# Optimization experiments

Hardware: AMD Instinct MI355X
Metric: run time of the kernel (lower is better)

Reference implementation:

```python
import jax, jax.numpy as jnp
import numpy as np

B, N, F_IN, F, H, K = 4, 128, 16, 64, 4, 50
C = F * H            # n_coefficients = hidden * n_heads
DEPTH, STEPS = 2, 3
L = 2 * DEPTH        # stacked flow layers: [xv0, vx0, xv1, vx1]
EPS = 1e-5

PARAM_NAMES = ["emb1_w", "emb1_b", "emb2_w", "emb2_b",
               "edge_in_w", "edge_in_b", "rbf_means", "rbf_betas",
               "edge_out1_w", "edge_out1_b", "edge_out2_w", "edge_out2_b",
               "xmix_w", "post1_w", "post1_b", "post2_w", "post2_b",
               "sem_w", "sem_b", "node1_w", "node1_b", "node2_w", "node2_b",
               "vel1_w", "vel1_b", "vel2_w", "coord1_w", "coord1_b", "coord2_w"]


def _lin(x, w, b=None):
    y = x @ w
    return y if b is None else y + b


def _pair_cat(h):
    # h_cat_ht: [B,N,N,2F], entry (i,j) = concat(h_i, h_j)
    return jnp.concatenate([jnp.broadcast_to(h[:, :, None, :], (B, N, N, F)),
                            jnp.broadcast_to(h[:, None, :, :], (B, N, N, F))], -1)


def _mp(p, i, h, x):
    dx = x[:, :, None, :] - x[:, None, :, :]                       # [B,N,N,3] x_i - x_j
    dn = jnp.sqrt(jnp.sum(dx * dx, -1, keepdims=True) + EPS * EPS)  # [B,N,N,1]
    hh = _pair_cat(h)                                              # [B,N,N,2F]
    # edge model: continuous-filter conv with concatenation (ExpNormal RBF smearing)
    hk = _lin(hh, p["edge_in_w"][i], p["edge_in_b"][i])            # [B,N,N,K]
    smear = jnp.exp(-p["rbf_betas"][i] * (jnp.exp(-dn) - p["rbf_means"][i]) ** 2)
    z = jnp.concatenate([hh, smear * hk, dn], -1)                  # [B,N,N,2F+K+1]
    he = _lin(jax.nn.silu(_lin(z, p["edge_out1_w"][i], p["edge_out1_b"][i])),
              p["edge_out2_w"][i], p["edge_out2_b"][i])            # [B,N,N,F]
    # spatial attention: mix unit displacement vectors with learned coefficients
    coeff = jnp.tanh(_lin(he, p["xmix_w"][i]))                     # [B,N,N,C]
    dxu = dx / (dn + EPS)
    comb = jnp.einsum('bijd,bijc->bicd', dxu, coeff) / N           # mean over j, [B,N,C,3]
    hc = jax.nn.silu(_lin(jnp.sum(comb * comb, -1), p["post1_w"][i], p["post1_b"][i]))
    hc = jax.nn.silu(_lin(hc, p["post2_w"][i], p["post2_b"][i]))   # [B,N,F]
    # semantic multi-head attention over neighbors j (self-edge masked)
    logits = jax.nn.celu(_lin(he, p["sem_w"][i], p["sem_b"][i]), alpha=2.0)  # [B,N,N,H]
    eye = jnp.eye(N, dtype=logits.dtype)[None, :, :, None]
    att = jax.nn.softmax(logits - 1e5 * eye, axis=-2)              # normalize over j
    # (h_e_mtx[...,None] * att[...,None,:]).flatten(-2,-1).sum(-2) without [B,N,N,F*H]
    h_e = jnp.einsum('bijf,bijh->bifh', he, att).reshape(B, N, C)  # [B,N,C]
    z = jnp.concatenate([h, h_e, hc], -1)                          # [B,N,F+C+F]
    out = jax.nn.silu(_lin(z, p["node1_w"][i], p["node1_b"][i]))
    out = jax.nn.silu(_lin(out, p["node2_w"][i], p["node2_b"][i]))
    return h + out                                                 # residual node update


def _flow(p, i, h, x, v):
    for _ in range(STEPS):
        h = _mp(p, i, h, x)
    hh = _pair_cat(h)
    dx = x[:, :, None, :] - x[:, None, :, :]
    c = _lin(jax.nn.silu(_lin(hh, p["coord1_w"][i], p["coord1_b"][i])), p["coord2_w"][i])
    delta_v = jnp.mean(c * dx, axis=-2)                            # [B,N,3]
    m = _lin(jax.nn.silu(_lin(h, p["vel1_w"][i], p["vel1_b"][i])), p["vel2_w"][i])  # [B,N,1]
    v = jnp.exp(m) * v
    log_det = jnp.sum(m, (-1, -2)) * 3.0                           # * v.shape[-1]
    v = delta_v + v
    x = x + v
    return x, v, log_det


def _forward(h, x, v, params):
    p = dict(zip(PARAM_NAMES, params))
    h = _lin(jax.nn.silu(_lin(h, p["emb1_w"], p["emb1_b"])), p["emb2_w"], p["emb2_b"])
    sld = jnp.zeros((B,), h.dtype)
    for d in range(DEPTH):
        x, v, ld = _flow(p, 2 * d, h, x, v)
        x = x - x.mean(-2, keepdims=True)
        v = v - v.mean(-2, keepdims=True)
        sld = sld + ld
        v, x, ld = _flow(p, 2 * d + 1, h, v, x)   # roles of x and v swapped
        x = x - x.mean(-2, keepdims=True)
        v = v - v.mean(-2, keepdims=True)
        sld = sld + ld
    return x, v, sld


def setup_inputs() -> dict:
    key = jax.random.key(0)
    ki = iter(jax.random.split(key, 40))
    def W(shape):
        fan = shape[-2] if len(shape) >= 2 else shape[-1]
        return jax.random.normal(next(ki), shape, jnp.float32) / np.float32(np.sqrt(fan))
    def Z(shape):
        return jnp.zeros(shape, jnp.float32)
    inp = {
        "h": jax.random.normal(next(ki), (B, N, F_IN), jnp.float32),
        "x": jax.random.normal(next(ki), (B, N, 3), jnp.float32),
        "v": jax.random.normal(next(ki), (B, N, 3), jnp.float32),
        "emb1_w": W((F_IN, F)), "emb1_b": Z((F,)),
        "emb2_w": W((F, F)), "emb2_b": Z((F,)),
        "edge_in_w": W((L, 2 * F, K)), "edge_in_b": Z((L, K)),
        "rbf_means": jnp.tile(jnp.linspace(np.float32(np.exp(-5.0)), 1.0, K, dtype=jnp.float32)[None], (L, 1)),
        "rbf_betas": jnp.full((L, K), np.float32(((2.0 / K) * (1.0 - np.exp(-5.0))) ** -2), jnp.float32),
        "edge_out1_w": W((L, 2 * F + K + 1, F)), "edge_out1_b": Z((L, F)),
        "edge_out2_w": W((L, F, F)), "edge_out2_b": Z((L, F)),
        "xmix_w": W((L, F, C)),
        "post1_w": W((L, C, F)), "post1_b": Z((L, F)),
        "post2_w": W((L, F, F)), "post2_b": Z((L, F)),
        "sem_w": W((L, F, H)), "sem_b": Z((L, H)),
        "node1_w": W((L, F + C + F, F)), "node1_b": Z((L, F)),
        "node2_w": W((L, F, F)), "node2_b": Z((L, F)),
        "vel1_w": W((L, F, F)), "vel1_b": Z((L, F)),
        "vel2_w": W((L, F, 1)),
        "coord1_w": W((L, 2 * F, F)), "coord1_b": Z((L, F)),
        "coord2_w": W((L, F, 1)),
    }
    return inp


def reference(h, x, v, emb1_w, emb1_b, emb2_w, emb2_b, edge_in_w, edge_in_b,
              rbf_means, rbf_betas, edge_out1_w, edge_out1_b, edge_out2_w, edge_out2_b,
              xmix_w, post1_w, post1_b, post2_w, post2_b, sem_w, sem_b,
              node1_w, node1_b, node2_w, node2_b, vel1_w, vel1_b, vel2_w,
              coord1_w, coord1_b, coord2_w):
    params = (emb1_w, emb1_b, emb2_w, emb2_b, edge_in_w, edge_in_b, rbf_means, rbf_betas,
              edge_out1_w, edge_out1_b, edge_out2_w, edge_out2_b, xmix_w,
              post1_w, post1_b, post2_w, post2_b, sem_w, sem_b,
              node1_w, node1_b, node2_w, node2_b, vel1_w, vel1_b, vel2_w,
              coord1_w, coord1_b, coord2_w)
    return _forward(h, x, v, params)
```

## Files before the change

### kernel.cpp

```cpp
#include <hip/hip_runtime.h>
#include <math.h>

namespace {

constexpr int B = 4, N = 128, FIN = 16, F = 64, H = 4, K = 50, C = 256;
constexpr int BN = B * N;
constexpr float EPS = 1e-5f;

typedef float v2f __attribute__((ext_vector_type(2)));
__device__ __forceinline__ v2f mk2(float a, float b) { v2f r; r.x = a; r.y = b; return r; }

__device__ __forceinline__ float silu_f(float x) { return x / (1.0f + __expf(-x)); }
__device__ __forceinline__ float tanh_f(float x) { return 1.0f - 2.0f / (__expf(2.0f * x) + 1.0f); }

__global__ void k_init(const float* __restrict__ x, const float* __restrict__ v,
                       float* __restrict__ xw, float* __restrict__ vw, float* __restrict__ sld) {
  int t = blockIdx.x * blockDim.x + threadIdx.x;
  if (t < B * N * 3) { xw[t] = x[t]; vw[t] = v[t]; }
  if (t < B) sld[t] = 0.0f;
}

__global__ __launch_bounds__(F) void k_embed(const float* __restrict__ hin,
    const float* __restrict__ w1, const float* __restrict__ b1,
    const float* __restrict__ w2, const float* __restrict__ b2, float* __restrict__ h0) {
  int node = blockIdx.x, f = threadIdx.x;
  __shared__ float t1[F];
  float acc = b1[f];
  #pragma unroll
  for (int r = 0; r < FIN; ++r) acc += hin[node * FIN + r] * w1[r * F + f];
  t1[f] = silu_f(acc);
  __syncthreads();
  float a0 = b2[f], a1 = 0.f, a2 = 0.f, a3 = 0.f;
  #pragma unroll
  for (int r = 0; r < F; r += 4) {
    a0 += t1[r] * w2[r * F + f];
    a1 += t1[r + 1] * w2[(r + 1) * F + f];
    a2 += t1[r + 2] * w2[(r + 2) * F + f];
    a3 += t1[r + 3] * w2[(r + 3) * F + f];
  }
  h0[node * F + f] = (a0 + a1) + (a2 + a3);
}

__global__ __launch_bounds__(256) void k_pre(const float* __restrict__ h0, float* __restrict__ hw,
    const float* __restrict__ ein_w, const float* __restrict__ eo1w,
    float* __restrict__ hkA, float* __restrict__ hkB,
    float* __restrict__ e1A, float* __restrict__ e1B) {
  int node = blockIdx.x, t = threadIdx.x;
  __shared__ float s_h[F];
  if (t < F) s_h[t] = h0[node * F + t];
  __syncthreads();
  if (t < F) hw[node * F + t] = s_h[t];
  if (t < 228) {
    v2f pa = mk2(0.f, 0.f), pb = mk2(0.f, 0.f);
    if (t < 50) { int k = t;
      #pragma unroll
      for (int r = 0; r < F; r += 4) {
        pa += mk2(s_h[r], s_h[r + 1]) * mk2(ein_w[r * K + k], ein_w[(r + 1) * K + k]);
        pb += mk2(s_h[r + 2], s_h[r + 3]) * mk2(ein_w[(r + 2) * K + k], ein_w[(r + 3) * K + k]);
      }
      hkA[node * K + k] = (pa.x + pb.x) + (pa.y + pb.y);
    } else if (t < 100) { int k = t - 50;
      #pragma unroll
      for (int r = 0; r < F; r += 4) {
        pa += mk2(s_h[r], s_h[r + 1]) * mk2(ein_w[(F + r) * K + k], ein_w[(F + r + 1) * K + k]);
        pb += mk2(s_h[r + 2], s_h[r + 3]) * mk2(ein_w[(F + r + 2) * K + k], ein_w[(F + r + 3) * K + k]);
      }
      hkB[node * K + k] = (pa.x + pb.x) + (pa.y + pb.y);
    } else if (t < 164) { int c = t - 100;
      #pragma unroll
      for (int r = 0; r < F; r += 4) {
        pa += mk2(s_h[r], s_h[r + 1]) * mk2(eo1w[r * F + c], eo1w[(r + 1) * F + c]);
        pb += mk2(s_h[r + 2], s_h[r + 3]) * mk2(eo1w[(r + 2) * F + c], eo1w[(r + 3) * F + c]);
      }
      e1A[node * F + c] = (pa.x + pb.x) + (pa.y + pb.y);
    } else { int c = t - 164;
      #pragma unroll
      for (int r = 0; r < F; r += 4) {
        pa += mk2(s_h[r], s_h[r + 1]) * mk2(eo1w[(F + r) * F + c], eo1w[(F + r + 1) * F + c]);
        pb += mk2(s_h[r + 2], s_h[r + 3]) * mk2(eo1w[(F + r + 2) * F + c], eo1w[(F + r + 3) * F + c]);
      }
      e1B[node * F + c] = (pa.x + pb.x) + (pa.y + pb.y);
    }
  }
}

__global__ __launch_bounds__(256, 2) void k_edge(
    const float* __restrict__ xp,
    const float* __restrict__ hkA_in, const float* __restrict__ hkB_in,
    const float* __restrict__ e1A_in, const float* __restrict__ e1B_in,
    const float* __restrict__ ein_b, const float* __restrict__ rbf_m, const float* __restrict__ rbf_b,
    const float* __restrict__ eo1w, const float* __restrict__ eo1b,
    const float* __restrict__ eo2w, const float* __restrict__ eo2b,
    const float* __restrict__ xmix,
    const float* __restrict__ semw, const float* __restrict__ semb,
    float* __restrict__ mS, float* __restrict__ Upart, float* __restrict__ combpart) {
  int blk = blockIdx.x;
  int b = blk >> 8, i = (blk >> 1) & 127, jh = blk & 1;
  int t = threadIdx.x, w = t >> 6, lane = t & 63;
  int bN = b * N;
  int bi2 = ((bN + i) << 1) + jh;

  __shared__ __align__(16) float s_heT[64 * 68];
  __shared__ __align__(16) float s_union[4352];
  __shared__ __align__(16) float4 s_dxn[64];
  __shared__ float s_inv[64];
  __shared__ float s_zkbase[K];
  __shared__ float s_e1base[F];
  __shared__ __align__(16) float s_zk[4][2][56];

  float* t1buf   = s_union;
  float* s_cpart = s_union;
  float* s_att   = s_union + 3072;

  if (t < K) s_zkbase[t] = hkA_in[(bN + i) * K + t] + ein_b[t];
  if (t >= 64 && t < 128) s_e1base[t - 64] = e1A_in[(bN + i) * F + (t - 64)] + eo1b[t - 64];
  if (lane >= 50 && lane < 56) { s_zk[w][0][lane] = 0.f; s_zk[w][1][lane] = 0.f; }
  if (t < 64) {
    const float* xb_ = xp + bN * 3;
    int jg = jh * 64 + t;
    float dx0 = xb_[i * 3 + 0] - xb_[jg * 3 + 0];
    float dx1 = xb_[i * 3 + 1] - xb_[jg * 3 + 1];
    float dx2 = xb_[i * 3 + 2] - xb_[jg * 3 + 2];
    float dn = sqrtf(dx0 * dx0 + dx1 * dx1 + dx2 * dx2 + EPS * EPS);
    s_dxn[t] = make_float4(dx0, dx1, dx2, dn);
    s_inv[t] = 1.0f / (dn + EPS);
  }
  __syncthreads();

  float rbm = 0.f, rbb = 0.f;
  if (lane < K) { rbm = rbf_m[lane]; rbb = rbf_b[lane]; }

  {
    int jbl = w * 16;
    int jbg = jh * 64 + jbl;
    {
      v2f wk2[26];
      #pragma unroll
      for (int k = 0; k < 25; ++k)
        wk2[k] = mk2(eo1w[(128 + 2 * k) * F + lane], eo1w[(128 + 2 * k + 1) * F + lane]);
      wk2[25] = mk2(0.f, 0.f);
      float w1d = eo1w[178 * F + lane];
      float e1b_lane = s_e1base[lane];
      float hk0 = (lane < K) ? hkB_in[(bN + jbg) * K + lane] : 0.f;
      float e1_c = e1B_in[(bN + jbg) * F + lane];
      if (lane < K) {
        float dn0 = s_dxn[jbl].w;
        float e = __expf(-dn0) - rbm;
        s_zk[w][0][lane] = __expf(-rbb * e * e) * (s_zkbase[lane] + hk0);
      }
      float hk_n = (lane < K) ? hkB_in[(bN + jbg + 1) * K + lane] : 0.f;
      float e1_n = e1B_in[(bN + jbg + 1) * F + lane];
      for (int jj = 0; jj < 16; ++jj) {
        int jl = jbl + jj;
        int cur = jj & 1;
        if (jj < 15) {
          if (lane < K) {
            float dn1 = s_dxn[jl + 1].w;
            float e = __expf(-dn1) - rbm;
            s_zk[w][cur ^ 1][lane] = __expf(-rbb * e * e) * (s_zkbase[lane] + hk_n);
          }
        }
        float e1v = e1_c;
        if (jj < 14) {
          hk_n = (lane < K) ? hkB_in[(bN + jbg + jj + 2) * K + lane] : 0.f;
          e1_c = e1_n;
          e1_n = e1B_in[(bN + jbg + jj + 2) * F + lane];
        } else {
          e1_c = e1_n;
        }
        float dn = s_dxn[jl].w;
        v2f pa = mk2(0.f, 0.f), pb = mk2(0.f, 0.f);
        const float4* z4 = (const float4*)(&s_zk[w][cur][0]);
        #pragma unroll
        for (int k4 = 0; k4 < 13; ++k4) {
          float4 z = z4[k4];
          pa += mk2(z.x, z.y) * wk2[2 * k4];
          pb += mk2(z.z, z.w) * wk2[2 * k4 + 1];
        }
        float base_ = e1b_lane + e1v + dn * w1d;
        float sum = base_ + ((pa.x + pb.x) + (pa.y + pb.y));
        t1buf[jl * 68 + lane] = silu_f(sum);
      }
    }
    {
      v2f er2[32];
      #pragma unroll
      for (int r = 0; r < 32; ++r)
        er2[r] = mk2(eo2w[(2 * r) * F + lane], eo2w[(2 * r + 1) * F + lane]);
      float b2 = eo2b[lane];
      for (int jj4 = 0; jj4 < 4; ++jj4) {
        float hv[4];
        #pragma unroll
        for (int q = 0; q < 4; ++q) {
          const float4* t4 = (const float4*)(&t1buf[(jbl + jj4 * 4 + q) * 68]);
          v2f pa = mk2(0.f, 0.f), pb = mk2(0.f, 0.f);
          #pragma unroll
          for (int r4 = 0; r4 < 16; ++r4) {
            float4 tt = t4[r4];
            pa += mk2(tt.x, tt.y) * er2[2 * r4];
            pb += mk2(tt.z, tt.w) * er2[2 * r4 + 1];
          }
          hv[q] = b2 + ((pa.x + pb.x) + (pa.y + pb.y));
        }
        *(float4*)(&s_heT[lane * 68 + jbl + jj4 * 4]) = make_float4(hv[0], hv[1], hv[2], hv[3]);
      }
    }
  }
  __syncthreads();

  {
    int c0 = 4 * (t & 63);
    v2f aX = mk2(0.f, 0.f), aXh = mk2(0.f, 0.f);
    v2f aY = mk2(0.f, 0.f), aYh = mk2(0.f, 0.f);
    v2f aZ = mk2(0.f, 0.f), aZh = mk2(0.f, 0.f);
    #pragma unroll 1
    for (int p = 0; p < 2; ++p) {
      int j0 = w * 16 + p * 8;
      v2f caccL[8], caccH[8];
      #pragma unroll
      for (int jj = 0; jj < 8; ++jj) { caccL[jj] = mk2(0.f, 0.f); caccH[jj] = mk2(0.f, 0.f); }
      for (int r = 0; r < 64; ++r) {
        float4 xm4 = *(const float4*)(&xmix[r * C + c0]);
        v2f xmL = mk2(xm4.x, xm4.y), xmH = mk2(xm4.z, xm4.w);
        const float4* hb = (const float4*)(&s_heT[r * 68 + j0]);
        float4 h0v = hb[0], h1v = hb[1];
#define CSTEP(idx, hval) \
        caccL[idx] += xmL * (hval); caccH[idx] += xmH * (hval);
        CSTEP(0, h0v.x)  CSTEP(1, h0v.y)  CSTEP(2, h0v.z)  CSTEP(3, h0v.w)
        CSTEP(4, h1v.x)  CSTEP(5, h1v.y)  CSTEP(6, h1v.z)  CSTEP(7, h1v.w)
#undef CSTEP
      }
      #pragma unroll
      for (int jj = 0; jj < 8; ++jj) {
        int jl = j0 + jj;
        float4 dq = s_dxn[jl];
        float inv = s_inv[jl];
        float s0 = tanh_f(caccL[jj].x) * inv;
        float s1 = tanh_f(caccL[jj].y) * inv;
        float s2 = tanh_f(caccH[jj].x) * inv;
        float s3 = tanh_f(caccH[jj].y) * inv;
        v2f s01 = mk2(s0, s1), s23 = mk2(s2, s3);
        aX  += s01 * dq.x; aXh += s23 * dq.x;
        aY  += s01 * dq.y; aYh += s23 * dq.y;
        aZ  += s01 * dq.z; aZh += s23 * dq.z;
      }
    }
    int cb = w * 768 + c0 * 3;
    s_cpart[cb + 0] = aX.x;  s_cpart[cb + 1]  = aY.x;  s_cpart[cb + 2]  = aZ.x;
    s_cpart[cb + 3] = aX.y;  s_cpart[cb + 4]  = aY.y;  s_cpart[cb + 5]  = aZ.y;
    s_cpart[cb + 6] = aXh.x; s_cpart[cb + 7]  = aYh.x; s_cpart[cb + 8]  = aZh.x;
    s_cpart[cb + 9] = aXh.y; s_cpart[cb + 10] = aYh.y; s_cpart[cb + 11] = aZh.y;
  }
  __syncthreads();

  {
    int c = t;
    float q0 = s_cpart[c * 3 + 0] + s_cpart[768 + c * 3 + 0] + s_cpart[1536 + c * 3 + 0] + s_cpart[2304 + c * 3 + 0];
    float q1 = s_cpart[c * 3 + 1] + s_cpart[768 + c * 3 + 1] + s_cpart[1536 + c * 3 + 1] + s_cpart[2304 + c * 3 + 1];
    float q2 = s_cpart[c * 3 + 2] + s_cpart[768 + c * 3 + 2] + s_cpart[1536 + c * 3 + 2] + s_cpart[2304 + c * 3 + 2];
    combpart[bi2 * 768 + c * 3 + 0] = q0;
    combpart[bi2 * 768 + c * 3 + 1] = q1;
    combpart[bi2 * 768 + c * 3 + 2] = q2;
  }

  {
    int jl = t & 63, hh = w;
    int jg = jh * 64 + jl;
    v2f lacc = mk2(0.f, 0.f);
    #pragma unroll 8
    for (int r = 0; r < 64; r += 2) {
      float hv0 = s_heT[r * 68 + jl];
      float hv1 = s_heT[(r + 1) * 68 + jl];
      lacc += mk2(hv0, hv1) * mk2(semw[r * H + hh], semw[(r + 1) * H + hh]);
    }
    float lg = semb[hh] + lacc.x + lacc.y;
    lg = lg > 0.f ? lg : 2.0f * (__expf(0.5f * lg) - 1.0f);
    if (jg == i) lg -= 1e5f;
    float m = lg;
    #pragma unroll
    for (int off = 32; off > 0; off >>= 1) m = fmaxf(m, __shfl_xor(m, off));
    float e = __expf(lg - m);
    float S = e;
    #pragma unroll
    for (int off = 32; off > 0; off >>= 1) S += __shfl_xor(S, off);
    s_att[hh * 64 + jl] = e;
    if (lane == 0) { mS[bi2 * 8 + hh * 2] = m; mS[bi2 * 8 + hh * 2 + 1] = S; }
  }
  __syncthreads();

  {
    int f = t >> 2, hh = t & 3;
    const float4* hr = (const float4*)(&s_heT[f * 68]);
    const float4* ar = (const float4*)(&s_att[hh * 64]);
    v2f pa = mk2(0.f, 0.f), pb = mk2(0.f, 0.f);
    #pragma unroll 8
    for (int jg4 = 0; jg4 < 16; ++jg4) {
      float4 hv = hr[jg4];
      float4 av = ar[jg4];
      pa += mk2(hv.x, hv.y) * mk2(av.x, av.y);
      pb += mk2(hv.z, hv.w) * mk2(av.z, av.w);
    }
    Upart[bi2 * 256 + t] = (pa.x + pb.x) + (pa.y + pb.y);
  }
}

template<int PRE, int TAIL>
__global__ __launch_bounds__(256, 2) void k_comb(
    float* __restrict__ hw,
    const float* __restrict__ mS, const float* __restrict__ Upart, const float* __restrict__ combpart,
    const float* __restrict__ p1w, const float* __restrict__ p1b,
    const float* __restrict__ p2w, const float* __restrict__ p2b,
    const float* __restrict__ n1w, const float* __restrict__ n1b,
    const float* __restrict__ n2w, const float* __restrict__ n2b,
    const float* __restrict__ ein_w, const float* __restrict__ eo1w,
    float* __restrict__ hkA_out, float* __restrict__ hkB_out,
    float* __restrict__ e1A_out, float* __restrict__ e1B_out,
    const float* __restrict__ c1w, const float* __restrict__ v1w, const float* __restrict__ v1b,
    const float* __restrict__ v2w,
    float* __restrict__ uA, float* __restrict__ uB, float* __restrict__ mbuf) {
  int blk = blockIdx.x, b = blk >> 7, i = blk & 127;
  int t = threadIdx.x, w = t >> 6, lane = t & 63;
  int bN = b * N;
  int bi2 = (bN + i) << 1;
  constexpr float invN = 1.0f / (float)N;

  __shared__ float s_hcin[C];
  __shared__ float s_cat[384];
  __shared__ float s_part[4][F];
  __shared__ float s_vec[F];
  __shared__ float s_hnew[F];

  float hi_val = (t < F) ? hw[(bN + i) * F + t] : 0.f;

  {
    int hh = t & 3;
    float m0 = mS[bi2 * 8 + hh * 2],       S0 = mS[bi2 * 8 + hh * 2 + 1];
    float m1 = mS[(bi2 + 1) * 8 + hh * 2], S1 = mS[(bi2 + 1) * 8 + hh * 2 + 1];
    float m = fmaxf(m0, m1);
    float w0 = __expf(m0 - m), w1 = __expf(m1 - m);
    float u = w0 * Upart[bi2 * 256 + t] + w1 * Upart[(bi2 + 1) * 256 + t];
    s_cat[64 + t] = u / (w0 * S0 + w1 * S1);
  }
  {
    int c = t;
    float q0 = (combpart[bi2 * 768 + c * 3 + 0] + combpart[(bi2 + 1) * 768 + c * 3 + 0]) * invN;
    float q1 = (combpart[bi2 * 768 + c * 3 + 1] + combpart[(bi2 + 1) * 768 + c * 3 + 1]) * invN;
    float q2 = (combpart[bi2 * 768 + c * 3 + 2] + combpart[(bi2 + 1) * 768 + c * 3 + 2]) * invN;
    s_hcin[c] = q0 * q0 + q1 * q1 + q2 * q2;
  }
  __syncthreads();

  {
    int c0 = w * 64;
    v2f pa = mk2(0.f, 0.f), pb = mk2(0.f, 0.f);
    #pragma unroll 8
    for (int cc = 0; cc < 64; cc += 4) {
      pa += mk2(s_hcin[c0 + cc], s_hcin[c0 + cc + 1])
          * mk2(p1w[(c0 + cc) * F + lane], p1w[(c0 + cc + 1) * F + lane]);
      pb += mk2(s_hcin[c0 + cc + 2], s_hcin[c0 + cc + 3])
          * mk2(p1w[(c0 + cc + 2) * F + lane], p1w[(c0 + cc + 3) * F + lane]);
    }
    s_part[w][lane] = (pa.x + pb.x) + (pa.y + pb.y);
  }
  __syncthreads();
  if (t < F) s_vec[t] = silu_f(s_part[0][t] + s_part[1][t] + s_part[2][t] + s_part[3][t] + p1b[t]);
  __syncthreads();
  if (t < F) {
    v2f pa = mk2(0.f, 0.f), pb = mk2(0.f, 0.f);
    #pragma unroll 8
    for (int r = 0; r < F; r += 4) {
      pa += mk2(s_vec[r], s_vec[r + 1]) * mk2(p2w[r * F + t], p2w[(r + 1) * F + t]);
      pb += mk2(s_vec[r + 2], s_vec[r + 3]) * mk2(p2w[(r + 2) * F + t], p2w[(r + 3) * F + t]);
    }
    s_cat[t] = hi_val;
    s_cat[320 + t] = silu_f(p2b[t] + (pa.x + pb.x) + (pa.y + pb.y));
  }
  __syncthreads();
  {
    int r0 = w * 96;
    v2f pa = mk2(0.f, 0.f), pb = mk2(0.f, 0.f);
    #pragma unroll 8
    for (int rr = 0; rr < 96; rr += 4) {
      pa += mk2(s_cat[r0 + rr], s_cat[r0 + rr + 1])
          * mk2(n1w[(r0 + rr) * F + lane], n1w[(r0 + rr + 1) * F + lane]);
      pb += mk2(s_cat[r0 + rr + 2], s_cat[r0 + rr + 3])
          * mk2(n1w[(r0 + rr + 2) * F + lane], n1w[(r0 + rr + 3) * F + lane]);
    }
    s_part[w][lane] = (pa.x + pb.x) + (pa.y + pb.y);
  }
  __syncthreads();
  if (t < F) s_vec[t] = silu_f(s_part[0][t] + s_part[1][t] + s_part[2][t] + s_part[3][t] + n1b[t]);
  __syncthreads();
  if (t < F) {
    v2f pa = mk2(0.f, 0.f), pb = mk2(0.f, 0.f);
    #pragma unroll 8
    for (int r = 0; r < F; r += 4) {
      pa += mk2(s_vec[r], s_vec[r + 1]) * mk2(n2w[r * F + t], n2w[(r + 1) * F + t]);
      pb += mk2(s_vec[r + 2], s_vec[r + 3]) * mk2(n2w[(r + 2) * F + t], n2w[(r + 3) * F + t]);
    }
    float hn = hi_val + silu_f(n2b[t] + (pa.x + pb.x) + (pa.y + pb.y));
    s_hnew[t] = hn;
    hw[(bN + i) * F + t] = hn;
  }
  __syncthreads();

  if (PRE) {
    if (t < 228) {
      v2f pa = mk2(0.f, 0.f), pb = mk2(0.f, 0.f);
      if (t < 50) { int k = t;
        #pragma unroll
        for (int r = 0; r < F; r += 4) {
          pa += mk2(s_hnew[r], s_hnew[r + 1]) * mk2(ein_w[r * K + k], ein_w[(r + 1) * K + k]);
          pb += mk2(s_hnew[r + 2], s_hnew[r + 3]) * mk2(ein_w[(r + 2) * K + k], ein_w[(r + 3) * K + k]);
        }
        hkA_out[(bN + i) * K + k] = (pa.x + pb.x) + (pa.y + pb.y);
      } else if (t < 100) { int k = t - 50;
        #pragma unroll
        for (int r = 0; r < F; r += 4) {
          pa += mk2(s_hnew[r], s_hnew[r + 1]) * mk2(ein_w[(F + r) * K + k], ein_w[(F + r + 1) * K + k]);
          pb += mk2(s_hnew[r + 2], s_hnew[r + 3]) * mk2(ein_w[(F + r + 2) * K + k], ein_w[(F + r + 3) * K + k]);
        }
        hkB_out[(bN + i) * K + k] = (pa.x + pb.x) + (pa.y + pb.y);
      } else if (t < 164) { int c = t - 100;
        #pragma unroll
        for (int r = 0; r < F; r += 4) {
          pa += mk2(s_hnew[r], s_hnew[r + 1]) * mk2(eo1w[r * F + c], eo1w[(r + 1) * F + c]);
          pb += mk2(s_hnew[r + 2], s_hnew[r + 3]) * mk2(eo1w[(r + 2) * F + c], eo1w[(r + 3) * F + c]);
        }
        e1A_out[(bN + i) * F + c] = (pa.x + pb.x) + (pa.y + pb.y);
      } else { int c = t - 164;
        #pragma unroll
        for (int r = 0; r < F; r += 4) {
          pa += mk2(s_hnew[r], s_hnew[r + 1]) * mk2(eo1w[(F + r) * F + c], eo1w[(F + r + 1) * F + c]);
          pb += mk2(s_hnew[r + 2], s_hnew[r + 3]) * mk2(eo1w[(F + r + 2) * F + c], eo1w[(F + r + 3) * F + c]);
        }
        e1B_out[(bN + i) * F + c] = (pa.x + pb.x) + (pa.y + pb.y);
      }
    }
  }
  if (TAIL) {
    if (w == 0) {
      v2f pa = mk2(0.f, 0.f), pb = mk2(0.f, 0.f);
      #pragma unroll
      for (int r = 0; r < F; r += 4) {
        pa += mk2(s_hnew[r], s_hnew[r + 1]) * mk2(c1w[r * F + lane], c1w[(r + 1) * F + lane]);
        pb += mk2(s_hnew[r + 2], s_hnew[r + 3]) * mk2(c1w[(r + 2) * F + lane], c1w[(r + 3) * F + lane]);
      }
      uA[(bN + i) * F + lane] = (pa.x + pb.x) + (pa.y + pb.y);
    } else if (w == 1) {
      v2f pa = mk2(0.f, 0.f), pb = mk2(0.f, 0.f);
      #pragma unroll
      for (int r = 0; r < F; r += 4) {
        pa += mk2(s_hnew[r], s_hnew[r + 1]) * mk2(c1w[(F + r) * F + lane], c1w[(F + r + 1) * F + lane]);
        pb += mk2(s_hnew[r + 2], s_hnew[r + 3]) * mk2(c1w[(F + r + 2) * F + lane], c1w[(F + r + 3) * F + lane]);
      }
      uB[(bN + i) * F + lane] = (pa.x + pb.x) + (pa.y + pb.y);
    } else if (w == 2) {
      v2f pa = mk2(0.f, 0.f), pb = mk2(0.f, 0.f);
      #pragma unroll
      for (int r = 0; r < F; r += 4) {
        pa += mk2(s_hnew[r], s_hnew[r + 1]) * mk2(v1w[r * F + lane], v1w[(r + 1) * F + lane]);
        pb += mk2(s_hnew[r + 2], s_hnew[r + 3]) * mk2(v1w[(r + 2) * F + lane], v1w[(r + 3) * F + lane]);
      }
      float tv = silu_f(v1b[lane] + (pa.x + pb.x) + (pa.y + pb.y)) * v2w[lane];
      #pragma unroll
      for (int off = 32; off > 0; off >>= 1) tv += __shfl_down(tv, off);
      if (lane == 0) mbuf[bN + i] = tv;
    }
  }
}

__global__ __launch_bounds__(256) void k_tail(const float* __restrict__ xb,
    const float* __restrict__ uA, const float* __restrict__ uB,
    const float* __restrict__ c1b, const float* __restrict__ c2w,
    float* __restrict__ dv) {
  int blk = blockIdx.x, b = blk >> 7, i = blk & 127;
  int t = threadIdx.x, w = t >> 6, lane = t & 63;
  __shared__ float s_xpos[N * 3];
  __shared__ float s_uAi[F];
  __shared__ float s_acc[4][3];
  for (int idx = t; idx < N * 3; idx += 256) s_xpos[idx] = xb[b * N * 3 + idx];
  if (t < F) s_uAi[t] = uA[(b * N + i) * F + t];
  __syncthreads();
  float xi0 = s_xpos[i * 3 + 0], xi1 = s_xpos[i * 3 + 1], xi2 = s_xpos[i * 3 + 2];
  float base = s_uAi[lane] + c1b[lane];
  float c2v = c2w[lane];
  float a0 = 0.f, a1 = 0.f, a2 = 0.f;
  for (int jj = 0; jj < 32; ++jj) {
    int j = w + 4 * jj;
    float tv = silu_f(base + uB[(b * N + j) * F + lane]) * c2v;
    #pragma unroll
    for (int off = 32; off > 0; off >>= 1) tv += __shfl_down(tv, off);
    if (lane == 0) {
      float dx0 = xi0 - s_xpos[j * 3 + 0];
      float dx1 = xi1 - s_xpos[j * 3 + 1];
      float dx2 = xi2 - s_xpos[j * 3 + 2];
      a0 += tv * dx0; a1 += tv * dx1; a2 += tv * dx2;
    }
  }
  if (lane == 0) { s_acc[w][0] = a0; s_acc[w][1] = a1; s_acc[w][2] = a2; }
  __syncthreads();
  if (t < 3) {
    float s = s_acc[0][t] + s_acc[1][t] + s_acc[2][t] + s_acc[3][t];
    dv[(b * N + i) * 3 + t] = s * (1.0f / (float)N);
  }
}

__global__ __launch_bounds__(128) void k_fin(float* __restrict__ xb, float* __restrict__ vb,
    const float* __restrict__ dv, const float* __restrict__ mbuf, float* __restrict__ sld) {
  int b = blockIdx.x, t = threadIdx.x;
  __shared__ float red[N];
  float m = mbuf[b * N + t];
  float em = __expf(m);
  float vv[3], xx[3];
  #pragma unroll
  for (int d = 0; d < 3; ++d) {
    int idx = (b * N + t) * 3 + d;
    vv[d] = em * vb[idx] + dv[idx];
    xx[d] = xb[idx] + vv[d];
  }
  #pragma unroll
  for (int d = 0; d < 3; ++d) {
    red[t] = xx[d];
    __syncthreads();
    for (int s = 64; s > 0; s >>= 1) { if (t < s) red[t] += red[t + s]; __syncthreads(); }
    xx[d] -= red[0] * (1.0f / (float)N);
    __syncthreads();
    red[t] = vv[d];
    __syncthreads();
    for (int s = 64; s > 0; s >>= 1) { if (t < s) red[t] += red[t + s]; __syncthreads(); }
    vv[d] -= red[0] * (1.0f / (float)N);
    __syncthreads();
  }
  #pragma unroll
  for (int d = 0; d < 3; ++d) {
    int idx = (b * N + t) * 3 + d;
    xb[idx] = xx[d];
    vb[idx] = vv[d];
  }
  red[t] = m;
  __syncthreads();
  for (int s = 64; s > 0; s >>= 1) { if (t < s) red[t] += red[t + s]; __syncthreads(); }
  if (t == 0) sld[b] += 3.0f * red[0];
}

__global__ void k_out(const float* __restrict__ xw, const float* __restrict__ vw,
                      const float* __restrict__ sld, float* __restrict__ out) {
  int t = blockIdx.x * blockDim.x + threadIdx.x;
  if (t < B * N * 3) { out[t] = xw[t]; out[B * N * 3 + t] = vw[t]; }
  if (t < B) out[2 * B * N * 3 + t] = sld[t];
}

}

extern "C" void kernel_launch(void* const* d_in, const int* in_sizes, int n_in,
                              void* d_out, int out_size, void* d_ws, size_t ws_size,
                              hipStream_t stream) {
  const float* in_h   = (const float*)d_in[0];
  const float* in_x   = (const float*)d_in[1];
  const float* in_v   = (const float*)d_in[2];
  const float* emb1_w = (const float*)d_in[3];
  const float* emb1_b = (const float*)d_in[4];
  const float* emb2_w = (const float*)d_in[5];
  const float* emb2_b = (const float*)d_in[6];
  const float* ein_w  = (const float*)d_in[7];
  const float* ein_b  = (const float*)d_in[8];
  const float* rbf_m  = (const float*)d_in[9];
  const float* rbf_b  = (const float*)d_in[10];
  const float* eo1w   = (const float*)d_in[11];
  const float* eo1b   = (const float*)d_in[12];
  const float* eo2w   = (const float*)d_in[13];
  const float* eo2b   = (const float*)d_in[14];
  const float* xmix   = (const float*)d_in[15];
  const float* p1w    = (const float*)d_in[16];
  const float* p1b    = (const float*)d_in[17];
  const float* p2w    = (const float*)d_in[18];
  const float* p2b    = (const float*)d_in[19];
  const float* semw   = (const float*)d_in[20];
  const float* semb   = (const float*)d_in[21];
  const float* n1w    = (const float*)d_in[22];
  const float* n1b    = (const float*)d_in[23];
  const float* n2w    = (const float*)d_in[24];
  const float* n2b    = (const float*)d_in[25];
  const float* v1w    = (const float*)d_in[26];
  const float* v1b    = (const float*)d_in[27];
  const float* v2w    = (const float*)d_in[28];
  const float* c1w    = (const float*)d_in[29];
  const float* c1b    = (const float*)d_in[30];
  const float* c2w    = (const float*)d_in[31];

  float* ws   = (float*)d_ws;
  float* h0   = ws;
  float* hw   = h0 + BN * F;
  float* hkA0 = hw + BN * F;
  float* hkB0 = hkA0 + BN * K;
  float* e1A0 = hkB0 + BN * K;
  float* e1B0 = e1A0 + BN * F;
  float* hkA1 = e1B0 + BN * F;
  float* hkB1 = hkA1 + BN * K;
  float* e1A1 = hkB1 + BN * K;
  float* e1B1 = e1A1 + BN * F;
  float* uA   = e1B1 + BN * F;
  float* uB   = uA + BN * F;
  float* xw   = uB + BN * F;
  float* vw   = xw + BN * 3;
  float* dvb  = vw + BN * 3;
  float* mbuf = dvb + BN * 3;
  float* sld  = mbuf + BN;
  float* mS   = sld + B;
  float* Up   = mS + BN * 2 * 8;
  float* cp   = Up + BN * 2 * 256;

  k_init<<<6, 256, 0, stream>>>(in_x, in_v, xw, vw, sld);
  k_embed<<<BN, F, 0, stream>>>(in_h, emb1_w, emb1_b, emb2_w, emb2_b, h0);

  float* hkA[2] = {hkA0, hkA1};
  float* hkB[2] = {hkB0, hkB1};
  float* e1A[2] = {e1A0, e1A1};
  float* e1B[2] = {e1B0, e1B1};

  for (int dep = 0; dep < 2; ++dep) {
    for (int half = 0; half < 2; ++half) {
      int l = 2 * dep + half;
      float* xb = half ? vw : xw;
      float* vb = half ? xw : vw;
      const float* einw_l = ein_w + l * 2 * F * K;
      const float* einb_l = ein_b + l * K;
      const float* rbm_l  = rbf_m + l * K;
      const float* rbb_l  = rbf_b + l * K;
      const float* eo1w_l = eo1w + l * 179 * F;
      const float* eo1b_l = eo1b + l * F;
      const float* eo2w_l = eo2w + l * F * F;
      const float* eo2b_l = eo2b + l * F;
      const float* xmix_l = xmix + l * F * C;
      const float* p1w_l  = p1w + l * C * F;
      const float* p1b_l  = p1b + l * F;
      const float* p2w_l  = p2w + l * F * F;
      const float* p2b_l  = p2b + l * F;
      const float* semw_l = semw + l * F * H;
      const float* semb_l = semb + l * H;
      const float* n1w_l  = n1w + l * 384 * F;
      const float* n1b_l  = n1b + l * F;
      const float* n2w_l  = n2w + l * F * F;
      const float* n2b_l  = n2b + l * F;
      const float* v1w_l  = v1w + l * F * F;
      const float* v1b_l  = v1b + l * F;
      const float* v2w_l  = v2w + l * F;
      const float* c1w_l  = c1w + l * 2 * F * F;
      const float* c1b_l  = c1b + l * F;
      const float* c2w_l  = c2w + l * F;

      k_pre<<<BN, 256, 0, stream>>>(h0, hw, einw_l, eo1w_l, hkA[0], hkB[0], e1A[0], e1B[0]);
      k_edge<<<BN * 2, 256, 0, stream>>>(xb, hkA[0], hkB[0], e1A[0], e1B[0],
          einb_l, rbm_l, rbb_l, eo1w_l, eo1b_l, eo2w_l, eo2b_l, xmix_l, semw_l, semb_l,
          mS, Up, cp);
      k_comb<1, 0><<<BN, 256, 0, stream>>>(hw, mS, Up, cp,
          p1w_l, p1b_l, p2w_l, p2b_l, n1w_l, n1b_l, n2w_l, n2b_l,
          einw_l, eo1w_l, hkA[1], hkB[1], e1A[1], e1B[1],
          c1w_l, v1w_l, v1b_l, v2w_l, uA, uB, mbuf);
      k_edge<<<BN * 2, 256, 0, stream>>>(xb, hkA[1], hkB[1], e1A[1], e1B[1],
          einb_l, rbm_l, rbb_l, eo1w_l, eo1b_l, eo2w_l, eo2b_l, xmix_l, semw_l, semb_l,
          mS, Up, cp);
      k_comb<1, 0><<<BN, 256, 0, stream>>>(hw, mS, Up, cp,
          p1w_l, p1b_l, p2w_l, p2b_l, n1w_l, n1b_l, n2w_l, n2b_l,
          einw_l, eo1w_l, hkA[0], hkB[0], e1A[0], e1B[0],
          c1w_l, v1w_l, v1b_l, v2w_l, uA, uB, mbuf);
      k_edge<<<BN * 2, 256, 0, stream>>>(xb, hkA[0], hkB[0], e1A[0], e1B[0],
          einb_l, rbm_l, rbb_l, eo1w_l, eo1b_l, eo2w_l, eo2b_l, xmix_l, semw_l, semb_l,
          mS, Up, cp);
      k_comb<0, 1><<<BN, 256, 0, stream>>>(hw, mS, Up, cp,
          p1w_l, p1b_l, p2w_l, p2b_l, n1w_l, n1b_l, n2w_l, n2b_l,
          einw_l, eo1w_l, hkA[1], hkB[1], e1A[1], e1B[1],
          c1w_l, v1w_l, v1b_l, v2w_l, uA, uB, mbuf);
      k_tail<<<BN, 256, 0, stream>>>(xb, uA, uB, c1b_l, c2w_l, dvb);
      k_fin<<<B, 128, 0, stream>>>(xb, vb, dvb, mbuf, sld);
    }
  }
  k_out<<<6, 256, 0, stream>>>(xw, vw, sld, (float*)d_out);
}
```

Measured before the change: 916.6 us.

## Split edge kernel over four j-quarters per node instead of two

```diff
diff --git a/kernel.cpp b/kernel.cpp
--- a/kernel.cpp
+++ b/kernel.cpp
@@ -95,29 +95,30 @@
     const float* __restrict__ semw, const float* __restrict__ semb,
     float* __restrict__ mS, float* __restrict__ Upart, float* __restrict__ combpart) {
   int blk = blockIdx.x;
-  int b = blk >> 8, i = (blk >> 1) & 127, jh = blk & 1;
+  int b = blk >> 9, i = (blk >> 2) & 127, jq = blk & 3;
   int t = threadIdx.x, w = t >> 6, lane = t & 63;
   int bN = b * N;
-  int bi2 = ((bN + i) << 1) + jh;
-
-  __shared__ __align__(16) float s_heT[64 * 68];
-  __shared__ __align__(16) float s_union[4352];
-  __shared__ __align__(16) float4 s_dxn[64];
-  __shared__ float s_inv[64];
+  int bi4 = ((bN + i) << 2) + jq;
+  int jgbase = jq * 32;
+
+  __shared__ __align__(16) float s_heT[64 * 36];
+  __shared__ __align__(16) float s_union[2176];
+  __shared__ __align__(16) float4 s_dxn[32];
+  __shared__ float s_inv[32];
   __shared__ float s_zkbase[K];
   __shared__ float s_e1base[F];
-  __shared__ __align__(16) float s_zk[4][2][56];
-
-  float* t1buf   = s_union;
-  float* s_cpart = s_union;
-  float* s_att   = s_union + 3072;
+  __shared__ __align__(16) float s_zk[4][56];
+
+  float* t1buf  = s_union;
+  float* s_comb = s_union;
+  float* s_att  = s_union + 768;
 
   if (t < K) s_zkbase[t] = hkA_in[(bN + i) * K + t] + ein_b[t];
   if (t >= 64 && t < 128) s_e1base[t - 64] = e1A_in[(bN + i) * F + (t - 64)] + eo1b[t - 64];
-  if (lane >= 50 && lane < 56) { s_zk[w][0][lane] = 0.f; s_zk[w][1][lane] = 0.f; }
-  if (t < 64) {
+  if (lane >= 50 && lane < 56) s_zk[w][lane] = 0.f;
+  if (t < 32) {
     const float* xb_ = xp + bN * 3;
-    int jg = jh * 64 + t;
+    int jg = jgbase + t;
     float dx0 = xb_[i * 3 + 0] - xb_[jg * 3 + 0];
     float dx1 = xb_[i * 3 + 1] - xb_[jg * 3 + 1];
     float dx2 = xb_[i * 3 + 2] - xb_[jg * 3 + 2];
@@ -131,8 +132,8 @@
   if (lane < K) { rbm = rbf_m[lane]; rbb = rbf_b[lane]; }
 
   {
-    int jbl = w * 16;
-    int jbg = jh * 64 + jbl;
+    int jbl = w * 8;
+    int nb = bN + jgbase + jbl;
     {
       v2f wk2[26];
       #pragma unroll
@@ -141,45 +142,31 @@
       wk2[25] = mk2(0.f, 0.f);
       float w1d = eo1w[178 * F + lane];
       float e1b_lane = s_e1base[lane];
-      float hk0 = (lane < K) ? hkB_in[(bN + jbg) * K + lane] : 0.f;
-      float e1_c = e1B_in[(bN + jbg) * F + lane];
-      if (lane < K) {
-        float dn0 = s_dxn[jbl].w;
-        float e = __expf(-dn0) - rbm;
-        s_zk[w][0][lane] = __expf(-rbb * e * e) * (s_zkbase[lane] + hk0);
-      }
-      float hk_n = (lane < K) ? hkB_in[(bN + jbg + 1) * K + lane] : 0.f;
-      float e1_n = e1B_in[(bN + jbg + 1) * F + lane];
-      for (int jj = 0; jj < 16; ++jj) {
+      float hk_c = (lane < K) ? hkB_in[nb * K + lane] : 0.f;
+      float e1_c = e1B_in[nb * F + lane];
+      for (int jj = 0; jj < 8; ++jj) {
         int jl = jbl + jj;
-        int cur = jj & 1;
-        if (jj < 15) {
-          if (lane < K) {
-            float dn1 = s_dxn[jl + 1].w;
-            float e = __expf(-dn1) - rbm;
-            s_zk[w][cur ^ 1][lane] = __expf(-rbb * e * e) * (s_zkbase[lane] + hk_n);
-          }
-        }
-        float e1v = e1_c;
-        if (jj < 14) {
-          hk_n = (lane < K) ? hkB_in[(bN + jbg + jj + 2) * K + lane] : 0.f;
-          e1_c = e1_n;
-          e1_n = e1B_in[(bN + jbg + jj + 2) * F + lane];
-        } else {
-          e1_c = e1_n;
+        float hk_n = 0.f, e1_n = 0.f;
+        if (jj < 7) {
+          hk_n = (lane < K) ? hkB_in[(nb + jj + 1) * K + lane] : 0.f;
+          e1_n = e1B_in[(nb + jj + 1) * F + lane];
         }
         float dn = s_dxn[jl].w;
+        if (lane < K) {
+          float e = __expf(-dn) - rbm;
+          s_zk[w][lane] = __expf(-rbb * e * e) * (s_zkbase[lane] + hk_c);
+        }
         v2f pa = mk2(0.f, 0.f), pb = mk2(0.f, 0.f);
-        const float4* z4 = (const float4*)(&s_zk[w][cur][0]);
+        const float4* z4 = (const float4*)(&s_zk[w][0]);
         #pragma unroll
         for (int k4 = 0; k4 < 13; ++k4) {
           float4 z = z4[k4];
           pa += mk2(z.x, z.y) * wk2[2 * k4];
           pb += mk2(z.z, z.w) * wk2[2 * k4 + 1];
         }
-        float base_ = e1b_lane + e1v + dn * w1d;
-        float sum = base_ + ((pa.x + pb.x) + (pa.y + pb.y));
-        t1buf[jl * 68 + lane] = silu_f(sum);
+        float base_ = e1b_lane + e1_c + dn * w1d;
+        t1buf[jl * 68 + lane] = silu_f(base_ + ((pa.x + pb.x) + (pa.y + pb.y)));
+        hk_c = hk_n; e1_c = e1_n;
       }
     }
     {
@@ -188,7 +175,7 @@
       for (int r = 0; r < 32; ++r)
         er2[r] = mk2(eo2w[(2 * r) * F + lane], eo2w[(2 * r + 1) * F + lane]);
       float b2 = eo2b[lane];
-      for (int jj4 = 0; jj4 < 4; ++jj4) {
+      for (int jj4 = 0; jj4 < 2; ++jj4) {
         float hv[4];
         #pragma unroll
         for (int q = 0; q < 4; ++q) {
@@ -202,75 +189,70 @@
           }
           hv[q] = b2 + ((pa.x + pb.x) + (pa.y + pb.y));
         }
-        *(float4*)(&s_heT[lane * 68 + jbl + jj4 * 4]) = make_float4(hv[0], hv[1], hv[2], hv[3]);
-      }
-    }
-  }
+        *(float4*)(&s_heT[lane * 36 + jbl + jj4 * 4]) = make_float4(hv[0], hv[1], hv[2], hv[3]);
+      }
+    }
+  }
+  __syncthreads();
+  for (int idx = t; idx < 768; idx += 256) s_comb[idx] = 0.f;
   __syncthreads();
 
   {
     int c0 = 4 * (t & 63);
+    int j0 = w * 8;
+    v2f caccL[8], caccH[8];
+    #pragma unroll
+    for (int jj = 0; jj < 8; ++jj) { caccL[jj] = mk2(0.f, 0.f); caccH[jj] = mk2(0.f, 0.f); }
+    for (int r = 0; r < 64; ++r) {
+      float4 xm4 = *(const float4*)(&xmix[r * C + c0]);
+      v2f xmL = mk2(xm4.x, xm4.y), xmH = mk2(xm4.z, xm4.w);
+      const float4* hb = (const float4*)(&s_heT[r * 36 + j0]);
+      float4 h0v = hb[0], h1v = hb[1];
+#define CSTEP(idx, hval) \
+      caccL[idx] += xmL * (hval); caccH[idx] += xmH * (hval);
+      CSTEP(0, h0v.x)  CSTEP(1, h0v.y)  CSTEP(2, h0v.z)  CSTEP(3, h0v.w)
+      CSTEP(4, h1v.x)  CSTEP(5, h1v.y)  CSTEP(6, h1v.z)  CSTEP(7, h1v.w)
+#undef CSTEP
+    }
     v2f aX = mk2(0.f, 0.f), aXh = mk2(0.f, 0.f);
     v2f aY = mk2(0.f, 0.f), aYh = mk2(0.f, 0.f);
     v2f aZ = mk2(0.f, 0.f), aZh = mk2(0.f, 0.f);
-    #pragma unroll 1
-    for (int p = 0; p < 2; ++p) {
-      int j0 = w * 16 + p * 8;
-      v2f caccL[8], caccH[8];
-      #pragma unroll
-      for (int jj = 0; jj < 8; ++jj) { caccL[jj] = mk2(0.f, 0.f); caccH[jj] = mk2(0.f, 0.f); }
-      for (int r = 0; r < 64; ++r) {
-        float4 xm4 = *(const float4*)(&xmix[r * C + c0]);
-        v2f xmL = mk2(xm4.x, xm4.y), xmH = mk2(xm4.z, xm4.w);
-        const float4* hb = (const float4*)(&s_heT[r * 68 + j0]);
-        float4 h0v = hb[0], h1v = hb[1];
-#define CSTEP(idx, hval) \
-        caccL[idx] += xmL * (hval); caccH[idx] += xmH * (hval);
-        CSTEP(0, h0v.x)  CSTEP(1, h0v.y)  CSTEP(2, h0v.z)  CSTEP(3, h0v.w)
-        CSTEP(4, h1v.x)  CSTEP(5, h1v.y)  CSTEP(6, h1v.z)  CSTEP(7, h1v.w)
-#undef CSTEP
-      }
-      #pragma unroll
-      for (int jj = 0; jj < 8; ++jj) {
-        int jl = j0 + jj;
-        float4 dq = s_dxn[jl];
-        float inv = s_inv[jl];
-        float s0 = tanh_f(caccL[jj].x) * inv;
-        float s1 = tanh_f(caccL[jj].y) * inv;
-        float s2 = tanh_f(caccH[jj].x) * inv;
-        float s3 = tanh_f(caccH[jj].y) * inv;
-        v2f s01 = mk2(s0, s1), s23 = mk2(s2, s3);
-        aX  += s01 * dq.x; aXh += s23 * dq.x;
-        aY  += s01 * dq.y; aYh += s23 * dq.y;
-        aZ  += s01 * dq.z; aZh += s23 * dq.z;
-      }
-    }
-    int cb = w * 768 + c0 * 3;
-    s_cpart[cb + 0] = aX.x;  s_cpart[cb + 1]  = aY.x;  s_cpart[cb + 2]  = aZ.x;
-    s_cpart[cb + 3] = aX.y;  s_cpart[cb + 4]  = aY.y;  s_cpart[cb + 5]  = aZ.y;
-    s_cpart[cb + 6] = aXh.x; s_cpart[cb + 7]  = aYh.x; s_cpart[cb + 8]  = aZh.x;
-    s_cpart[cb + 9] = aXh.y; s_cpart[cb + 10] = aYh.y; s_cpart[cb + 11] = aZh.y;
-  }
-  __syncthreads();
-
-  {
-    int c = t;
-    float q0 = s_cpart[c * 3 + 0] + s_cpart[768 + c * 3 + 0] + s_cpart[1536 + c * 3 + 0] + s_cpart[2304 + c * 3 + 0];
-    float q1 = s_cpart[c * 3 + 1] + s_cpart[768 + c * 3 + 1] + s_cpart[1536 + c * 3 + 1] + s_cpart[2304 + c * 3 + 1];
-    float q2 = s_cpart[c * 3 + 2] + s_cpart[768 + c * 3 + 2] + s_cpart[1536 + c * 3 + 2] + s_cpart[2304 + c * 3 + 2];
-    combpart[bi2 * 768 + c * 3 + 0] = q0;
-    combpart[bi2 * 768 + c * 3 + 1] = q1;
-    combpart[bi2 * 768 + c * 3 + 2] = q2;
-  }
-
-  {
-    int jl = t & 63, hh = w;
-    int jg = jh * 64 + jl;
+    #pragma unroll
+    for (int jj = 0; jj < 8; ++jj) {
+      int jl = j0 + jj;
+      float4 dq = s_dxn[jl];
+      float inv = s_inv[jl];
+      float s0 = tanh_f(caccL[jj].x) * inv;
+      float s1 = tanh_f(caccL[jj].y) * inv;
+      float s2 = tanh_f(caccH[jj].x) * inv;
+      float s3 = tanh_f(caccH[jj].y) * inv;
+      v2f s01 = mk2(s0, s1), s23 = mk2(s2, s3);
+      aX  += s01 * dq.x; aXh += s23 * dq.x;
+      aY  += s01 * dq.y; aYh += s23 * dq.y;
+      aZ  += s01 * dq.z; aZh += s23 * dq.z;
+    }
+    atomicAdd(&s_comb[(c0 + 0) * 3 + 0], aX.x);
+    atomicAdd(&s_comb[(c0 + 0) * 3 + 1], aY.x);
+    atomicAdd(&s_comb[(c0 + 0) * 3 + 2], aZ.x);
+    atomicAdd(&s_comb[(c0 + 1) * 3 + 0], aX.y);
+    atomicAdd(&s_comb[(c0 + 1) * 3 + 1], aY.y);
+    atomicAdd(&s_comb[(c0 + 1) * 3 + 2], aZ.y);
+    atomicAdd(&s_comb[(c0 + 2) * 3 + 0], aXh.x);
+    atomicAdd(&s_comb[(c0 + 2) * 3 + 1], aYh.x);
+    atomicAdd(&s_comb[(c0 + 2) * 3 + 2], aZh.x);
+    atomicAdd(&s_comb[(c0 + 3) * 3 + 0], aXh.y);
+    atomicAdd(&s_comb[(c0 + 3) * 3 + 1], aYh.y);
+    atomicAdd(&s_comb[(c0 + 3) * 3 + 2], aZh.y);
+  }
+
+  if (t < 128) {
+    int jl = t & 31, hh = t >> 5;
+    int jg = jgbase + jl;
     v2f lacc = mk2(0.f, 0.f);
     #pragma unroll 8
     for (int r = 0; r < 64; r += 2) {
-      float hv0 = s_heT[r * 68 + jl];
-      float hv1 = s_heT[(r + 1) * 68 + jl];
+      float hv0 = s_heT[r * 36 + jl];
+      float hv1 = s_heT[(r + 1) * 36 + jl];
       lacc += mk2(hv0, hv1) * mk2(semw[r * H + hh], semw[(r + 1) * H + hh]);
     }
     float lg = semb[hh] + lacc.x + lacc.y;
@@ -278,29 +260,35 @@
     if (jg == i) lg -= 1e5f;
     float m = lg;
     #pragma unroll
-    for (int off = 32; off > 0; off >>= 1) m = fmaxf(m, __shfl_xor(m, off));
+    for (int off = 16; off > 0; off >>= 1) m = fmaxf(m, __shfl_xor(m, off));
     float e = __expf(lg - m);
     float S = e;
     #pragma unroll
-    for (int off = 32; off > 0; off >>= 1) S += __shfl_xor(S, off);
-    s_att[hh * 64 + jl] = e;
-    if (lane == 0) { mS[bi2 * 8 + hh * 2] = m; mS[bi2 * 8 + hh * 2 + 1] = S; }
-  }
-  __syncthreads();
-
+    for (int off = 16; off > 0; off >>= 1) S += __shfl_xor(S, off);
+    s_att[hh * 32 + jl] = e;
+    if ((t & 31) == 0) { mS[bi4 * 8 + hh * 2] = m; mS[bi4 * 8 + hh * 2 + 1] = S; }
+  }
+  __syncthreads();
+
+  {
+    int c = t;
+    combpart[bi4 * 768 + c * 3 + 0] = s_comb[c * 3 + 0];
+    combpart[bi4 * 768 + c * 3 + 1] = s_comb[c * 3 + 1];
+    combpart[bi4 * 768 + c * 3 + 2] = s_comb[c * 3 + 2];
+  }
   {
     int f = t >> 2, hh = t & 3;
-    const float4* hr = (const float4*)(&s_heT[f * 68]);
-    const float4* ar = (const float4*)(&s_att[hh * 64]);
+    const float4* hr = (const float4*)(&s_heT[f * 36]);
+    const float4* ar = (const float4*)(&s_att[hh * 32]);
     v2f pa = mk2(0.f, 0.f), pb = mk2(0.f, 0.f);
-    #pragma unroll 8
-    for (int jg4 = 0; jg4 < 16; ++jg4) {
+    #pragma unroll
+    for (int jg4 = 0; jg4 < 8; ++jg4) {
       float4 hv = hr[jg4];
       float4 av = ar[jg4];
       pa += mk2(hv.x, hv.y) * mk2(av.x, av.y);
       pb += mk2(hv.z, hv.w) * mk2(av.z, av.w);
     }
-    Upart[bi2 * 256 + t] = (pa.x + pb.x) + (pa.y + pb.y);
+    Upart[bi4 * 256 + t] = (pa.x + pb.x) + (pa.y + pb.y);
   }
 }
 
@@ -321,7 +309,7 @@
   int blk = blockIdx.x, b = blk >> 7, i = blk & 127;
   int t = threadIdx.x, w = t >> 6, lane = t & 63;
   int bN = b * N;
-  int bi2 = (bN + i) << 1;
+  int bi4 = (bN + i) << 2;
   constexpr float invN = 1.0f / (float)N;
 
   __shared__ float s_hcin[C];
@@ -334,18 +322,32 @@
 
   {
     int hh = t & 3;
-    float m0 = mS[bi2 * 8 + hh * 2],       S0 = mS[bi2 * 8 + hh * 2 + 1];
-    float m1 = mS[(bi2 + 1) * 8 + hh * 2], S1 = mS[(bi2 + 1) * 8 + hh * 2 + 1];
-    float m = fmaxf(m0, m1);
-    float w0 = __expf(m0 - m), w1 = __expf(m1 - m);
-    float u = w0 * Upart[bi2 * 256 + t] + w1 * Upart[(bi2 + 1) * 256 + t];
-    s_cat[64 + t] = u / (w0 * S0 + w1 * S1);
+    float mk[4], Sk[4];
+    #pragma unroll
+    for (int k = 0; k < 4; ++k) {
+      mk[k] = mS[(bi4 + k) * 8 + hh * 2];
+      Sk[k] = mS[(bi4 + k) * 8 + hh * 2 + 1];
+    }
+    float m = fmaxf(fmaxf(mk[0], mk[1]), fmaxf(mk[2], mk[3]));
+    float u = 0.f, S = 0.f;
+    #pragma unroll
+    for (int k = 0; k < 4; ++k) {
+      float wk = __expf(mk[k] - m);
+      u += wk * Upart[(bi4 + k) * 256 + t];
+      S += wk * Sk[k];
+    }
+    s_cat[64 + t] = u / S;
   }
   {
     int c = t;
-    float q0 = (combpart[bi2 * 768 + c * 3 + 0] + combpart[(bi2 + 1) * 768 + c * 3 + 0]) * invN;
-    float q1 = (combpart[bi2 * 768 + c * 3 + 1] + combpart[(bi2 + 1) * 768 + c * 3 + 1]) * invN;
-    float q2 = (combpart[bi2 * 768 + c * 3 + 2] + combpart[(bi2 + 1) * 768 + c * 3 + 2]) * invN;
+    float q0 = 0.f, q1 = 0.f, q2 = 0.f;
+    #pragma unroll
+    for (int k = 0; k < 4; ++k) {
+      q0 += combpart[(bi4 + k) * 768 + c * 3 + 0];
+      q1 += combpart[(bi4 + k) * 768 + c * 3 + 1];
+      q2 += combpart[(bi4 + k) * 768 + c * 3 + 2];
+    }
+    q0 *= invN; q1 *= invN; q2 *= invN;
     s_hcin[c] = q0 * q0 + q1 * q1 + q2 * q2;
   }
   __syncthreads();
@@ -608,8 +610,8 @@
   float* mbuf = dvb + BN * 3;
   float* sld  = mbuf + BN;
   float* mS   = sld + B;
-  float* Up   = mS + BN * 2 * 8;
-  float* cp   = Up + BN * 2 * 256;
+  float* Up   = mS + BN * 4 * 8;
+  float* cp   = Up + BN * 4 * 256;
 
   k_init<<<6, 256, 0, stream>>>(in_x, in_v, xw, vw, sld);
   k_embed<<<BN, F, 0, stream>>>(in_h, emb1_w, emb1_b, emb2_w, emb2_b, h0);
@@ -651,21 +653,21 @@
       const float* c2w_l  = c2w + l * F;
 
       k_pre<<<BN, 256, 0, stream>>>(h0, hw, einw_l, eo1w_l, hkA[0], hkB[0], e1A[0], e1B[0]);
-      k_edge<<<BN * 2, 256, 0, stream>>>(xb, hkA[0], hkB[0], e1A[0], e1B[0],
+      k_edge<<<BN * 4, 256, 0, stream>>>(xb, hkA[0], hkB[0], e1A[0], e1B[0],
           einb_l, rbm_l, rbb_l, eo1w_l, eo1b_l, eo2w_l, eo2b_l, xmix_l, semw_l, semb_l,
           mS, Up, cp);
       k_comb<1, 0><<<BN, 256, 0, stream>>>(hw, mS, Up, cp,
           p1w_l, p1b_l, p2w_l, p2b_l, n1w_l, n1b_l, n2w_l, n2b_l,
           einw_l, eo1w_l, hkA[1], hkB[1], e1A[1], e1B[1],
           c1w_l, v1w_l, v1b_l, v2w_l, uA, uB, mbuf);
-      k_edge<<<BN * 2, 256, 0, stream>>>(xb, hkA[1], hkB[1], e1A[1], e1B[1],
+      k_edge<<<BN * 4, 256, 0, stream>>>(xb, hkA[1], hkB[1], e1A[1], e1B[1],
           einb_l, rbm_l, rbb_l, eo1w_l, eo1b_l, eo2w_l, eo2b_l, xmix_l, semw_l, semb_l,
           mS, Up, cp);
       k_comb<1, 0><<<BN, 256, 0, stream>>>(hw, mS, Up, cp,
           p1w_l, p1b_l, p2w_l, p2b_l, n1w_l, n1b_l, n2w_l, n2b_l,
           einw_l, eo1w_l, hkA[0], hkB[0], e1A[0], e1B[0],
           c1w_l, v1w_l, v1b_l, v2w_l, uA, uB, mbuf);
-      k_edge<<<BN * 2, 256, 0, stream>>>(xb, hkA[0], hkB[0], e1A[0], e1B[0],
+      k_edge<<<BN * 4, 256, 0, stream>>>(xb, hkA[0], hkB[0], e1A[0], e1B[0],
           einb_l, rbm_l, rbb_l, eo1w_l, eo1b_l, eo2w_l, eo2b_l, xmix_l, semw_l, semb_l,
           mS, Up, cp);
       k_comb<0, 1><<<BN, 256, 0, stream>>>(hw, mS, Up, cp,
```

Measured after the change: 1.431 ms. 1.56x slower.
